# Kernel optimization log

Hardware: AMD Instinct MI355X
Metric: run time of the kernel (lower is better)

The kernel has to match this reference:

```python
import jax, jax.numpy as jnp
import numpy as np

N_POINTS = 65536
DIM = 8
E0 = N_POINTS - 1      # H0 generators (edges killing components)
E1 = 2_000_000         # H1 generators (birth edge + death edge)


def setup_inputs() -> dict:
    key = jax.random.key(0)
    k1, k2, k3 = jax.random.split(key, 3)
    points = jax.random.normal(k1, (N_POINTS, DIM), dtype=jnp.float32)
    verts0 = jax.random.randint(k2, (E0, 2), 0, N_POINTS, dtype=jnp.int64)
    verts1 = jax.random.randint(k3, (E1, 4), 0, N_POINTS, dtype=jnp.int64)
    return {"points": points, "verts0": verts0, "verts1": verts1}


def reference(points, verts0, verts1):
    # H0 death times: distance between the two vertices of each killing edge.
    # deaths[i] = || points[verts0[i,0]] - points[verts0[i,1]] ||
    d0 = points[verts0[:, 0]] - points[verts0[:, 1]]        # [E0, D]
    deaths = jnp.linalg.norm(d0, axis=-1)                    # [E0]

    # H1 diagram: birth = ||p[v0]-p[v1]||, death = ||p[v2]-p[v3]||,
    # computed as paired gathers on columns (0,2) vs (1,3) like the original.
    a = points[verts1[:, jnp.array([0, 2])]]                 # [E1, 2, D]
    b = points[verts1[:, jnp.array([1, 3])]]                 # [E1, 2, D]
    dgm1 = jnp.linalg.norm(a - b, axis=-1)                   # [E1, 2]
    return deaths, dgm1
```

## Files before the change

kernel.cpp:

```cpp
#include <hip/hip_runtime.h>
#include <hip/hip_fp16.h>
#include <math.h>


__global__ __launch_bounds__(256) void cvt_kernel(
    const float* __restrict__ pts, __half* __restrict__ out, int n4) {
    int i = blockIdx.x * blockDim.x + threadIdx.x;
    if (i < n4) {
        float4 f = ((const float4*)pts)[i];
        __half2 h0 = __floats2half2_rn(f.x, f.y);
        __half2 h1 = __floats2half2_rn(f.z, f.w);
        ((__half2*)out)[2 * i]     = h0;
        ((__half2*)out)[2 * i + 1] = h1;
    }
}

__device__ __forceinline__ float2 u2f2(unsigned u) {
    __half2 h = *reinterpret_cast<__half2*>(&u);
    return __half22float2(h);
}

__device__ __forceinline__ float dist8h(const uint4* __restrict__ p, int ia, int ib) {
    uint4 a = p[ia];
    uint4 b = p[ib];
    float2 ax = u2f2(a.x), ay = u2f2(a.y), az = u2f2(a.z), aw = u2f2(a.w);
    float2 bx = u2f2(b.x), by = u2f2(b.y), bz = u2f2(b.z), bw = u2f2(b.w);
    float d0 = ax.x - bx.x, d1 = ax.y - bx.y;
    float d2 = ay.x - by.x, d3 = ay.y - by.y;
    float d4 = az.x - bz.x, d5 = az.y - bz.y;
    float d6 = aw.x - bw.x, d7 = aw.y - bw.y;
    float s = d0 * d0 + d1 * d1 + d2 * d2 + d3 * d3
            + d4 * d4 + d5 * d5 + d6 * d6 + d7 * d7;
    return sqrtf(s);
}

__global__ __launch_bounds__(256) void rips_kernel_h(
    const __half* __restrict__ points16,
    const int* __restrict__ verts0,
    const int* __restrict__ verts1,
    float* __restrict__ out,
    int e0, int e1) {
    int tid = blockIdx.x * blockDim.x + threadIdx.x;
    const uint4* p = (const uint4*)points16;
    if (tid < e1) {
        int4 v = ((const int4*)verts1)[tid];
        float r0 = dist8h(p, v.x, v.y);
        float r1 = dist8h(p, v.z, v.w);
        out[e0 + 2 * tid]     = r0;
        out[e0 + 2 * tid + 1] = r1;
    } else {
        int j = tid - e1;
        if (j < e0) {
            int2 v = ((const int2*)verts0)[j];
            out[j] = dist8h(p, v.x, v.y);
        }
    }
}

__device__ __forceinline__ float dist8f(const float4* __restrict__ p, int ia, int ib) {
    float4 a0 = p[2 * ia], a1 = p[2 * ia + 1];
    float4 b0 = p[2 * ib], b1 = p[2 * ib + 1];
    float d0 = a0.x - b0.x, d1 = a0.y - b0.y, d2 = a0.z - b0.z, d3 = a0.w - b0.w;
    float d4 = a1.x - b1.x, d5 = a1.y - b1.y, d6 = a1.z - b1.z, d7 = a1.w - b1.w;
    return sqrtf(d0*d0 + d1*d1 + d2*d2 + d3*d3 + d4*d4 + d5*d5 + d6*d6 + d7*d7);
}

__global__ __launch_bounds__(256) void rips_kernel_f(
    const float* __restrict__ points,
    const int* __restrict__ verts0,
    const int* __restrict__ verts1,
    float* __restrict__ out,
    int e0, int e1) {
    int tid = blockIdx.x * blockDim.x + threadIdx.x;
    const float4* p = (const float4*)points;
    if (tid < e1) {
        int4 v = ((const int4*)verts1)[tid];
        out[e0 + 2 * tid]     = dist8f(p, v.x, v.y);
        out[e0 + 2 * tid + 1] = dist8f(p, v.z, v.w);
    } else {
        int j = tid - e1;
        if (j < e0) {
            int2 v = ((const int2*)verts0)[j];
            out[j] = dist8f(p, v.x, v.y);
        }
    }
}

extern "C" void kernel_launch(void* const* d_in, const int* in_sizes, int n_in,
                              void* d_out, int out_size, void* d_ws, size_t ws_size,
                              hipStream_t stream) {
    const float* points = (const float*)d_in[0];
    const int* verts0   = (const int*)d_in[1];
    const int* verts1   = (const int*)d_in[2];
    float* out = (float*)d_out;

    int npts_flat = in_sizes[0];
    int e0 = in_sizes[1] / 2;
    int e1 = in_sizes[2] / 4;

    int total = e1 + e0;
    int block = 256;
    int grid = (total + block - 1) / block;

    size_t fp16_bytes = (size_t)npts_flat * sizeof(__half);
    if (ws_size >= fp16_bytes) {
        __half* p16 = (__half*)d_ws;
        int n4 = npts_flat / 4;
        cvt_kernel<<<(n4 + 255) / 256, 256, 0, stream>>>(points, p16, n4);
        rips_kernel_h<<<grid, block, 0, stream>>>(p16, verts0, verts1, out, e0, e1);
    } else {
        rips_kernel_f<<<grid, block, 0, stream>>>(points, verts0, verts1, out, e0, e1);
    }
}
```

Measured before the change: 115.8 us.

## Batch four H1 rows per thread with inline-asm sc0 gathers

Each H1 thread now handles four strided rows and issues eight 16-byte point gathers at a time through inline assembly carrying the sc0 cache-policy bit, followed by an explicit vmcnt wait. The goal is more memory-level parallelism per thread and control over cache behaviour for the random point gathers, which dominate the cost. In exchange the grid is four times smaller, the waitcnt(0) serialises the two gather batches, and the hand-written asm is fragile and bypasses compiler scheduling.

```diff
diff --git a/kernel.cpp b/kernel.cpp
--- a/kernel.cpp
+++ b/kernel.cpp
@@ -2,6 +2,9 @@
 #include <hip/hip_fp16.h>
 #include <math.h>
 
+
+typedef float vfloat4 __attribute__((ext_vector_type(4)));
+typedef unsigned int vuint4 __attribute__((ext_vector_type(4)));
 
 __global__ __launch_bounds__(256) void cvt_kernel(
     const float* __restrict__ pts, __half* __restrict__ out, int n4) {
@@ -15,42 +18,109 @@
     }
 }
 
+__device__ __forceinline__ void gather8_sc0(
+    const __half* __restrict__ base,
+    unsigned o0, unsigned o1, unsigned o2, unsigned o3,
+    unsigned o4, unsigned o5, unsigned o6, unsigned o7,
+    vuint4& r0, vuint4& r1, vuint4& r2, vuint4& r3,
+    vuint4& r4, vuint4& r5, vuint4& r6, vuint4& r7) {
+    asm volatile(
+        "global_load_dwordx4 %0, %8, %16 sc0\n\t"
+        "global_load_dwordx4 %1, %9, %16 sc0\n\t"
+        "global_load_dwordx4 %2, %10, %16 sc0\n\t"
+        "global_load_dwordx4 %3, %11, %16 sc0\n\t"
+        "global_load_dwordx4 %4, %12, %16 sc0\n\t"
+        "global_load_dwordx4 %5, %13, %16 sc0\n\t"
+        "global_load_dwordx4 %6, %14, %16 sc0\n\t"
+        "global_load_dwordx4 %7, %15, %16 sc0\n\t"
+        "s_waitcnt vmcnt(0)"
+        : "=&v"(r0), "=&v"(r1), "=&v"(r2), "=&v"(r3),
+          "=&v"(r4), "=&v"(r5), "=&v"(r6), "=&v"(r7)
+        : "v"(o0), "v"(o1), "v"(o2), "v"(o3),
+          "v"(o4), "v"(o5), "v"(o6), "v"(o7),
+          "s"(base)
+        : "memory");
+}
+
 __device__ __forceinline__ float2 u2f2(unsigned u) {
     __half2 h = *reinterpret_cast<__half2*>(&u);
     return __half22float2(h);
 }
 
-__device__ __forceinline__ float dist8h(const uint4* __restrict__ p, int ia, int ib) {
-    uint4 a = p[ia];
-    uint4 b = p[ib];
+__device__ __forceinline__ float dist8r(vuint4 a, vuint4 b) {
     float2 ax = u2f2(a.x), ay = u2f2(a.y), az = u2f2(a.z), aw = u2f2(a.w);
     float2 bx = u2f2(b.x), by = u2f2(b.y), bz = u2f2(b.z), bw = u2f2(b.w);
     float d0 = ax.x - bx.x, d1 = ax.y - bx.y;
     float d2 = ay.x - by.x, d3 = ay.y - by.y;
     float d4 = az.x - bz.x, d5 = az.y - bz.y;
     float d6 = aw.x - bw.x, d7 = aw.y - bw.y;
-    float s = d0 * d0 + d1 * d1 + d2 * d2 + d3 * d3
-            + d4 * d4 + d5 * d5 + d6 * d6 + d7 * d7;
-    return sqrtf(s);
+    return sqrtf(d0*d0 + d1*d1 + d2*d2 + d3*d3 + d4*d4 + d5*d5 + d6*d6 + d7*d7);
 }
 
-__global__ __launch_bounds__(256) void rips_kernel_h(
+__device__ __forceinline__ float dist8h(const vuint4* __restrict__ p, int ia, int ib) {
+    return dist8r(p[ia], p[ib]);
+}
+
+__global__ __launch_bounds__(256) void rips_kernel_sc0(
     const __half* __restrict__ points16,
     const int* __restrict__ verts0,
     const int* __restrict__ verts1,
     float* __restrict__ out,
-    int e0, int e1) {
+    int e0, int e1, int nh1) {
     int tid = blockIdx.x * blockDim.x + threadIdx.x;
-    const uint4* p = (const uint4*)points16;
-    if (tid < e1) {
-        int4 v = ((const int4*)verts1)[tid];
-        float r0 = dist8h(p, v.x, v.y);
-        float r1 = dist8h(p, v.z, v.w);
-        out[e0 + 2 * tid]     = r0;
-        out[e0 + 2 * tid + 1] = r1;
+    if (tid < nh1) {
+        const int4* v1 = (const int4*)verts1;
+        int r0 = tid;
+        int r1 = tid + nh1;
+        int r2 = tid + 2 * nh1;
+        int r3 = tid + 3 * nh1;
+        int4 a = v1[r0];
+        int4 b = (r1 < e1) ? v1[r1] : a;
+        int4 c = (r2 < e1) ? v1[r2] : a;
+        int4 d = (r3 < e1) ? v1[r3] : a;
+
+        vuint4 g0, g1, g2, g3, g4, g5, g6, g7;
+        gather8_sc0(points16,
+                    (unsigned)a.x << 4, (unsigned)a.y << 4,
+                    (unsigned)a.z << 4, (unsigned)a.w << 4,
+                    (unsigned)b.x << 4, (unsigned)b.y << 4,
+                    (unsigned)b.z << 4, (unsigned)b.w << 4,
+                    g0, g1, g2, g3, g4, g5, g6, g7);
+        {
+            float s0 = dist8r(g0, g1);
+            float s1 = dist8r(g2, g3);
+            float* o = out + e0 + 2 * r0;
+            o[0] = s0; o[1] = s1;
+        }
+        if (r1 < e1) {
+            float s0 = dist8r(g4, g5);
+            float s1 = dist8r(g6, g7);
+            float* o = out + e0 + 2 * r1;
+            o[0] = s0; o[1] = s1;
+        }
+
+        gather8_sc0(points16,
+                    (unsigned)c.x << 4, (unsigned)c.y << 4,
+                    (unsigned)c.z << 4, (unsigned)c.w << 4,
+                    (unsigned)d.x << 4, (unsigned)d.y << 4,
+                    (unsigned)d.z << 4, (unsigned)d.w << 4,
+                    g0, g1, g2, g3, g4, g5, g6, g7);
+        if (r2 < e1) {
+            float s0 = dist8r(g0, g1);
+            float s1 = dist8r(g2, g3);
+            float* o = out + e0 + 2 * r2;
+            o[0] = s0; o[1] = s1;
+        }
+        if (r3 < e1) {
+            float s0 = dist8r(g4, g5);
+            float s1 = dist8r(g6, g7);
+            float* o = out + e0 + 2 * r3;
+            o[0] = s0; o[1] = s1;
+        }
     } else {
-        int j = tid - e1;
+        int j = tid - nh1;
         if (j < e0) {
+            const vuint4* p = (const vuint4*)points16;
             int2 v = ((const int2*)verts0)[j];
             out[j] = dist8h(p, v.x, v.y);
         }
@@ -98,17 +168,21 @@
     int e0 = in_sizes[1] / 2;
     int e1 = in_sizes[2] / 4;
 
-    int total = e1 + e0;
-    int block = 256;
-    int grid = (total + block - 1) / block;
-
     size_t fp16_bytes = (size_t)npts_flat * sizeof(__half);
     if (ws_size >= fp16_bytes) {
         __half* p16 = (__half*)d_ws;
         int n4 = npts_flat / 4;
         cvt_kernel<<<(n4 + 255) / 256, 256, 0, stream>>>(points, p16, n4);
-        rips_kernel_h<<<grid, block, 0, stream>>>(p16, verts0, verts1, out, e0, e1);
+        int nh1 = (e1 + 3) / 4;
+        int total = nh1 + e0;
+        int block = 256;
+        int grid = (total + block - 1) / block;
+        rips_kernel_sc0<<<grid, block, 0, stream>>>(p16, verts0, verts1, out,
+                                                    e0, e1, nh1);
     } else {
+        int total = e1 + e0;
+        int block = 256;
+        int grid = (total + block - 1) / block;
         rips_kernel_f<<<grid, block, 0, stream>>>(points, verts0, verts1, out, e0, e1);
     }
 }
```

Measured after the change: 116.7 us. No clear change (+0.7%).
